# Optimization experiments

Measured on AMD Instinct MI355X. Metric: run time of the kernel, lower is better.

The kernel has to match this reference:

```python
import jax, jax.numpy as jnp
import numpy as np

KERNEL_MUL = 2.0
KERNEL_NUM = 5


def _index_matrix(b: int) -> jnp.ndarray:
    # non-linear JMMD index matrix (linear=False)
    im = np.zeros((2 * b, 2 * b), dtype=np.float32)
    off = 1.0 / float(b * (b - 1))
    eye = np.eye(b, dtype=bool)
    im[:b, :b][~eye] = off
    im[b:, b:][~eye] = off
    im[:b, b:] = -1.0 / float(b * b)
    im[b:, :b] = -1.0 / float(b * b)
    return jnp.asarray(im)


def _gaussian_kernel(source, target):
    total = jnp.concatenate([source, target], axis=0)  # [2b, d]
    n = total.shape[0]
    sq = jnp.sum(total * total, axis=1)  # [2b]
    # pairwise squared L2 via Gram matrix (same math as expand/diff/sum)
    l2 = sq[:, None] + sq[None, :] - 2.0 * (total @ total.T)
    l2 = jnp.maximum(l2, 0.0)
    # bandwidth computed on detached distances (torch uses .data)
    bw = jax.lax.stop_gradient(jnp.sum(l2)) / float(n * n - n)
    bw = bw / (KERNEL_MUL ** (KERNEL_NUM // 2))
    k = jnp.zeros_like(l2)
    for i in range(KERNEL_NUM):
        k = k + jnp.exp(-l2 / (bw * (KERNEL_MUL ** i)))
    return k


def setup_inputs() -> dict:
    key = jax.random.key(0)
    k1, k2, k3, k4 = jax.random.split(key, 4)
    b, d1, d2 = 2048, 4096, 2048
    return {
        "z1_s": jax.random.normal(k1, (b, d1), dtype=jnp.float32),
        "z1_t": jax.random.normal(k2, (b, d1), dtype=jnp.float32),
        "z2_s": jax.random.normal(k3, (b, d2), dtype=jnp.float32),
        "z2_t": jax.random.normal(k4, (b, d2), dtype=jnp.float32),
    }


def reference(z1_s, z1_t, z2_s, z2_t):
    b = z1_s.shape[0]
    index_matrix = _index_matrix(b)  # [2b, 2b]
    kernel_matrix = _gaussian_kernel(z1_s, z1_t) * _gaussian_kernel(z2_s, z2_t)
    loss = jnp.sum(kernel_matrix * index_matrix) + 2.0 / float(b - 1)
    return loss
```

## Files before the change

### kernel.cpp

```cpp
#include <hip/hip_runtime.h>
#include <cstdint>

#define NTOT 4096
#define BHALF 2048
#define D1 4096
#define D2 2048
#define TT 32
#define NTILES 528

typedef __attribute__((ext_vector_type(4))) float f32x4;
typedef __attribute__((ext_vector_type(4))) int i32x4;
typedef __attribute__((ext_vector_type(8))) int i32x8;

__device__ __forceinline__ void glds16(const uint8_t* g, uint8_t* l) {
    __builtin_amdgcn_global_load_lds(
        (const __attribute__((address_space(1))) void*)(uintptr_t)g,
        (__attribute__((address_space(3))) void*)(uint32_t)(uintptr_t)l,
        16, 0, 0);
}

__device__ __forceinline__ i32x4 ldsr(uint32_t addr) {
    i32x4 r;
    asm volatile("ds_read_b128 %0, %1" : "=v"(r) : "v"(addr));
    return r;
}

__device__ __forceinline__ float fp8dec(unsigned b) {
    unsigned e = (b >> 3) & 15u, m = b & 7u;
    float v = e ? __uint_as_float(((e + 120u) << 23) | (m << 20))
                : (float)m * 0.001953125f;
    return (b & 128u) ? -v : v;
}

__global__ void prep_kernel(const float* __restrict__ z1s, const float* __restrict__ z1t,
                            const float* __restrict__ z2s, const float* __restrict__ z2t,
                            float* __restrict__ sq1, float* __restrict__ sq2,
                            uint8_t* __restrict__ t1f8, uint8_t* __restrict__ t2f8,
                            float* __restrict__ s1, float* __restrict__ s2,
                            unsigned* __restrict__ ctrl, float* __restrict__ out) {
    int bid = blockIdx.x;
    int tid = threadIdx.x;
    if (bid == 0) { for (int i = tid; i < 4096; i += 256) s1[i] = 0.f; }
    if (bid == 1) { for (int i = tid; i < 2048; i += 256) s2[i] = 0.f; }
    if (bid == 2) {
        if (tid < 4) ctrl[tid] = 0u;
        if (tid == 4) out[0] = 2.0f / (float)(BHALF - 1);
    }
    int which = bid >> 12;
    int row = bid & 4095;
    int d = which ? D2 : D1;
    const float* s_ = which ? z2s : z1s;
    const float* t_ = which ? z2t : z1t;
    const float* src = (row < BHALF) ? s_ + (size_t)row * d : t_ + (size_t)(row - BHALF) * d;
    uint8_t* dst = (which ? t2f8 : t1f8) + (size_t)row * d;
    float* sq = which ? sq2 : sq1;
    const float4* src4 = (const float4*)src;
    float a = 0.f;
    int n8 = d >> 3;
    for (int i = tid; i < n8; i += 256) {
        float4 v0 = src4[2 * i], v1 = src4[2 * i + 1];
        a += v0.x * v0.x + v0.y * v0.y + v0.z * v0.z + v0.w * v0.w;
        a += v1.x * v1.x + v1.y * v1.y + v1.z * v1.z + v1.w * v1.w;
        int w0 = __builtin_amdgcn_cvt_pk_fp8_f32(v0.x, v0.y, 0, 0);
        w0 = __builtin_amdgcn_cvt_pk_fp8_f32(v0.z, v0.w, w0, 1);
        int w1 = __builtin_amdgcn_cvt_pk_fp8_f32(v1.x, v1.y, 0, 0);
        w1 = __builtin_amdgcn_cvt_pk_fp8_f32(v1.z, v1.w, w1, 1);
        ((uint2*)dst)[i] = uint2{(unsigned)w0, (unsigned)w1};
    }
    for (int o = 32; o; o >>= 1) a += __shfl_down(a, o);
    __shared__ float sh[4];
    int lane = tid & 63, w = tid >> 6;
    if (lane == 0) sh[w] = a;
    __syncthreads();
    if (tid == 0) sq[row] = sh[0] + sh[1] + sh[2] + sh[3];
}

__device__ __forceinline__ void gemm_mx_pipe(const uint8_t* __restrict__ ga,
                                             const uint8_t* __restrict__ gb,
                                             int d,
                                             uint8_t* A0, uint8_t* B0,
                                             uint8_t* A1, uint8_t* B1,
                                             f32x4 (&acc)[4][4], int wv, int lane,
                                             int wm, int wn, int lm, int quad) {
    int nsteps = d >> 7;
    int rsub = lane >> 3;
    int ql = (lane & 7) ^ rsub;
    const uint8_t* pa = ga + (size_t)(wv * 32 + rsub) * d + ql * 16;
    const uint8_t* pb = gb + (size_t)(wv * 32 + rsub) * d + ql * 16;
    uint8_t* dA[2] = { A0 + wv * 4096, A1 + wv * 4096 };
    uint8_t* dB[2] = { B0 + wv * 4096, B1 + wv * 4096 };
    uint32_t baseA[2] = { (uint32_t)(uintptr_t)A0, (uint32_t)(uintptr_t)A1 };
    uint32_t baseB[2] = { (uint32_t)(uintptr_t)B0, (uint32_t)(uintptr_t)B1 };
    int s0 = ((2 * quad) ^ (lm & 7)) * 16;
    int s1 = ((2 * quad + 1) ^ (lm & 7)) * 16;
    uint32_t offA[4], offB[4];
#pragma unroll
    for (int i = 0; i < 4; ++i) {
        offA[i] = (uint32_t)((wm * 64 + i * 16 + lm) * 128);
        offB[i] = (uint32_t)((wn * 64 + i * 16 + lm) * 128);
    }
#pragma unroll
    for (int i = 0; i < 4; ++i) {
        glds16(pa + (size_t)i * 8 * d, dA[0] + i * 1024);
        glds16(pb + (size_t)i * 8 * d, dB[0] + i * 1024);
    }
    for (int k = 0; k < nsteps; ++k) {
        int cur = k & 1, nxt = cur ^ 1;
        size_t koff = (size_t)((k + 1 < nsteps) ? (k + 1) : 0) << 7;
#pragma unroll
        for (int i = 0; i < 4; ++i) {
            glds16(pa + koff + (size_t)i * 8 * d, dA[nxt] + i * 1024);
            glds16(pb + koff + (size_t)i * 8 * d, dB[nxt] + i * 1024);
        }
        asm volatile("s_waitcnt vmcnt(8)\n\ts_barrier" ::: "memory");
        i32x4 b00 = ldsr(baseB[cur] + offB[0] + s0), b01 = ldsr(baseB[cur] + offB[0] + s1);
        i32x4 b10 = ldsr(baseB[cur] + offB[1] + s0), b11 = ldsr(baseB[cur] + offB[1] + s1);
        i32x4 a00 = ldsr(baseA[cur] + offA[0] + s0), a01 = ldsr(baseA[cur] + offA[0] + s1);
        i32x4 a10 = ldsr(baseA[cur] + offA[1] + s0), a11 = ldsr(baseA[cur] + offA[1] + s1);
        i32x4 b20 = ldsr(baseB[cur] + offB[2] + s0), b21 = ldsr(baseB[cur] + offB[2] + s1);
        i32x4 b30 = ldsr(baseB[cur] + offB[3] + s0), b31 = ldsr(baseB[cur] + offB[3] + s1);
        i32x4 a20 = ldsr(baseA[cur] + offA[2] + s0), a21 = ldsr(baseA[cur] + offA[2] + s1);
        i32x4 a30 = ldsr(baseA[cur] + offA[3] + s0), a31 = ldsr(baseA[cur] + offA[3] + s1);
        union F { i32x4 h[2]; i32x8 v; };
        F ua0, ua1, ua2, ua3, ub0, ub1, ub2, ub3;
        asm volatile("s_waitcnt lgkmcnt(8)"
                     : "+v"(b00), "+v"(b01), "+v"(b10), "+v"(b11),
                       "+v"(a00), "+v"(a01), "+v"(a10), "+v"(a11));
        __builtin_amdgcn_sched_barrier(0);
        ub0.h[0] = b00; ub0.h[1] = b01; ub1.h[0] = b10; ub1.h[1] = b11;
        ua0.h[0] = a00; ua0.h[1] = a01; ua1.h[0] = a10; ua1.h[1] = a11;
        __builtin_amdgcn_s_setprio(1);
        acc[0][0] = __builtin_amdgcn_mfma_scale_f32_16x16x128_f8f6f4(ua0.v, ub0.v, acc[0][0], 0, 0, 0, 0x7F7F7F7F, 0, 0x7F7F7F7F);
        acc[0][1] = __builtin_amdgcn_mfma_scale_f32_16x16x128_f8f6f4(ua0.v, ub1.v, acc[0][1], 0, 0, 0, 0x7F7F7F7F, 0, 0x7F7F7F7F);
        acc[1][0] = __builtin_amdgcn_mfma_scale_f32_16x16x128_f8f6f4(ua1.v, ub0.v, acc[1][0], 0, 0, 0, 0x7F7F7F7F, 0, 0x7F7F7F7F);
        acc[1][1] = __builtin_amdgcn_mfma_scale_f32_16x16x128_f8f6f4(ua1.v, ub1.v, acc[1][1], 0, 0, 0, 0x7F7F7F7F, 0, 0x7F7F7F7F);
        __builtin_amdgcn_s_setprio(0);
        asm volatile("s_waitcnt lgkmcnt(4)"
                     : "+v"(b20), "+v"(b21), "+v"(b30), "+v"(b31));
        __builtin_amdgcn_sched_barrier(0);
        ub2.h[0] = b20; ub2.h[1] = b21; ub3.h[0] = b30; ub3.h[1] = b31;
        __builtin_amdgcn_s_setprio(1);
        acc[0][2] = __builtin_amdgcn_mfma_scale_f32_16x16x128_f8f6f4(ua0.v, ub2.v, acc[0][2], 0, 0, 0, 0x7F7F7F7F, 0, 0x7F7F7F7F);
        acc[0][3] = __builtin_amdgcn_mfma_scale_f32_16x16x128_f8f6f4(ua0.v, ub3.v, acc[0][3], 0, 0, 0, 0x7F7F7F7F, 0, 0x7F7F7F7F);
        acc[1][2] = __builtin_amdgcn_mfma_scale_f32_16x16x128_f8f6f4(ua1.v, ub2.v, acc[1][2], 0, 0, 0, 0x7F7F7F7F, 0, 0x7F7F7F7F);
        acc[1][3] = __builtin_amdgcn_mfma_scale_f32_16x16x128_f8f6f4(ua1.v, ub3.v, acc[1][3], 0, 0, 0, 0x7F7F7F7F, 0, 0x7F7F7F7F);
        __builtin_amdgcn_s_setprio(0);
        asm volatile("s_waitcnt lgkmcnt(0)"
                     : "+v"(a20), "+v"(a21), "+v"(a30), "+v"(a31));
        __builtin_amdgcn_sched_barrier(0);
        asm volatile("s_barrier" ::: "memory");
        __builtin_amdgcn_sched_barrier(0);
        ua2.h[0] = a20; ua2.h[1] = a21; ua3.h[0] = a30; ua3.h[1] = a31;
        __builtin_amdgcn_s_setprio(1);
        acc[2][0] = __builtin_amdgcn_mfma_scale_f32_16x16x128_f8f6f4(ua2.v, ub0.v, acc[2][0], 0, 0, 0, 0x7F7F7F7F, 0, 0x7F7F7F7F);
        acc[2][1] = __builtin_amdgcn_mfma_scale_f32_16x16x128_f8f6f4(ua2.v, ub1.v, acc[2][1], 0, 0, 0, 0x7F7F7F7F, 0, 0x7F7F7F7F);
        acc[2][2] = __builtin_amdgcn_mfma_scale_f32_16x16x128_f8f6f4(ua2.v, ub2.v, acc[2][2], 0, 0, 0, 0x7F7F7F7F, 0, 0x7F7F7F7F);
        acc[2][3] = __builtin_amdgcn_mfma_scale_f32_16x16x128_f8f6f4(ua2.v, ub3.v, acc[2][3], 0, 0, 0, 0x7F7F7F7F, 0, 0x7F7F7F7F);
        acc[3][0] = __builtin_amdgcn_mfma_scale_f32_16x16x128_f8f6f4(ua3.v, ub0.v, acc[3][0], 0, 0, 0, 0x7F7F7F7F, 0, 0x7F7F7F7F);
        acc[3][1] = __builtin_amdgcn_mfma_scale_f32_16x16x128_f8f6f4(ua3.v, ub1.v, acc[3][1], 0, 0, 0, 0x7F7F7F7F, 0, 0x7F7F7F7F);
        acc[3][2] = __builtin_amdgcn_mfma_scale_f32_16x16x128_f8f6f4(ua3.v, ub2.v, acc[3][2], 0, 0, 0, 0x7F7F7F7F, 0, 0x7F7F7F7F);
        acc[3][3] = __builtin_amdgcn_mfma_scale_f32_16x16x128_f8f6f4(ua3.v, ub3.v, acc[3][3], 0, 0, 0, 0x7F7F7F7F, 0, 0x7F7F7F7F);
        __builtin_amdgcn_s_setprio(0);
    }
}

__global__ __launch_bounds__(256, 2) void jmmd_fused(
    const uint8_t* __restrict__ t1f8, const uint8_t* __restrict__ t2f8,
    const float* __restrict__ sq1, const float* __restrict__ sq2,
    float* __restrict__ s1v, float* __restrict__ s2v,
    unsigned* __restrict__ ctrl, float* __restrict__ out) {
    __shared__ alignas(16) uint8_t smem[4][16384];
    int tid = threadIdx.x;
    int bid = blockIdx.x;

    if (bid < 384) {
        int which = bid >= 256;
        int local = which ? bid - 256 : bid;
        int d = which ? D2 : D1;
        int colchunks = d >> 10;
        int cb = local % colchunks, rb = local / colchunks;
        const uint8_t* base = which ? t2f8 : t1f8;
        float* s = which ? s2v : s1v;
        int col = (cb << 10) + tid * 4;
        const uint8_t* p = base + (size_t)(rb * 64) * d + col;
        float a0 = 0.f, a1 = 0.f, a2 = 0.f, a3 = 0.f;
#pragma unroll 4
        for (int r = 0; r < 64; ++r) {
            uchar4 u = *(const uchar4*)(p + (size_t)r * d);
            a0 += fp8dec(u.x); a1 += fp8dec(u.y); a2 += fp8dec(u.z); a3 += fp8dec(u.w);
        }
        atomicAdd(&s[col], a0); atomicAdd(&s[col + 1], a1);
        atomicAdd(&s[col + 2], a2); atomicAdd(&s[col + 3], a3);
        __threadfence();
        __syncthreads();
        unsigned* rkp = (unsigned*)(smem[0] + 64);
        if (tid == 0) *rkp = atomicAdd(&ctrl[0], 1u);
        __syncthreads();
        unsigned rk = *rkp;
        __syncthreads();
        if (rk == 383u) {
            float a1_ = 0.f, a2_ = 0.f, q1_ = 0.f, q2_ = 0.f;
            for (int i = tid; i < 4096; i += 256) {
                float v = __uint_as_float(atomicOr((unsigned*)&s1v[i], 0u));
                a1_ += v * v; q1_ += sq1[i]; q2_ += sq2[i];
            }
            for (int i = tid; i < 2048; i += 256) {
                float v = __uint_as_float(atomicOr((unsigned*)&s2v[i], 0u));
                a2_ += v * v;
            }
            for (int o = 32; o; o >>= 1) {
                a1_ += __shfl_down(a1_, o); a2_ += __shfl_down(a2_, o);
                q1_ += __shfl_down(q1_, o); q2_ += __shfl_down(q2_, o);
            }
            float* fsh = (float*)smem[0];
            int lane = tid & 63, w = tid >> 6;
            if (lane == 0) { fsh[0 * 4 + w] = a1_; fsh[1 * 4 + w] = a2_; fsh[2 * 4 + w] = q1_; fsh[3 * 4 + w] = q2_; }
            __syncthreads();
            if (tid == 0) {
                double ss1 = (double)fsh[0] + fsh[1] + fsh[2] + fsh[3];
                double ss2 = (double)fsh[4] + fsh[5] + fsh[6] + fsh[7];
                double t1 = (double)fsh[8] + fsh[9] + fsh[10] + fsh[11];
                double t2 = (double)fsh[12] + fsh[13] + fsh[14] + fsh[15];
                double S1 = 2.0 * (double)NTOT * t1 - 2.0 * ss1;
                double S2 = 2.0 * (double)NTOT * t2 - 2.0 * ss2;
                const double L2E = 1.4426950408889634;
                double nn = (double)NTOT * (double)(NTOT - 1);
                atomicExch(&ctrl[2], __float_as_uint((float)(nn * L2E / (4.0 * S1))));
                atomicExch(&ctrl[3], __float_as_uint((float)(nn * L2E / (4.0 * S2))));
                __threadfence();
                atomicExch(&ctrl[1], 1u);
            }
            __syncthreads();
        }
    }

    int ti = 0, r = bid;
    while (r >= TT - ti) { r -= TT - ti; ++ti; }
    int tj = ti + r;
    int i0 = ti * 128, j0 = tj * 128;
    int lane = tid & 63, wv = tid >> 6;
    int wm = wv >> 1, wn = wv & 1, lm = lane & 15, quad = lane >> 4;
    f32x4 acc1[4][4] = {};
    f32x4 acc2[4][4] = {};
    gemm_mx_pipe(t1f8 + (size_t)i0 * D1, t1f8 + (size_t)j0 * D1, D1,
                 smem[0], smem[1], smem[2], smem[3], acc1, wv, lane, wm, wn, lm, quad);
    asm volatile("s_waitcnt vmcnt(0)\n\ts_barrier" ::: "memory");
    gemm_mx_pipe(t2f8 + (size_t)i0 * D2, t2f8 + (size_t)j0 * D2, D2,
                 smem[0], smem[1], smem[2], smem[3], acc2, wv, lane, wm, wn, lm, quad);
    asm volatile("s_waitcnt vmcnt(0)" ::: "memory");
    __syncthreads();

    float* cvp = (float*)smem[1];
    if (tid == 0) {
        while (atomicOr(&ctrl[1], 0u) == 0u) __builtin_amdgcn_s_sleep(8);
        cvp[0] = __uint_as_float(atomicOr(&ctrl[2], 0u));
        cvp[1] = __uint_as_float(atomicOr(&ctrl[3], 0u));
    }
    __syncthreads();
    float c1 = cvp[0], c2 = cvp[1];
    float local = 0.f;
    bool diag = (ti == tj);
#pragma unroll
    for (int mi = 0; mi < 4; ++mi) {
        int rbase = wm * 64 + mi * 16 + quad * 4;
#pragma unroll
        for (int ni = 0; ni < 4; ++ni) {
            int col = wn * 64 + ni * 16 + lm;
            float sb1 = sq1[j0 + col], sb2 = sq2[j0 + col];
#pragma unroll
            for (int rr = 0; rr < 4; ++rr) {
                int row = rbase + rr;
                float l2a = fmaxf(sq1[i0 + row] + sb1 - 2.f * acc1[mi][ni][rr], 0.f);
                float l2b = fmaxf(sq2[i0 + row] + sb2 - 2.f * acc2[mi][ni][rr], 0.f);
                float t1 = __builtin_amdgcn_exp2f(-l2a * c1);
                float k1 = t1; float u1 = t1 * t1; k1 += u1; u1 *= u1; k1 += u1; u1 *= u1; k1 += u1; u1 *= u1; k1 += u1;
                float t2 = __builtin_amdgcn_exp2f(-l2b * c2);
                float k2 = t2; float u2 = t2 * t2; k2 += u2; u2 *= u2; k2 += u2; u2 *= u2; k2 += u2; u2 *= u2; k2 += u2;
                float v = k1 * k2;
                if (diag && (row == col)) v = 0.f;
                local += v;
            }
        }
    }
    for (int o = 32; o; o >>= 1) local += __shfl_down(local, o);
    float* redp = (float*)smem[0];
    if (lane == 0) redp[wv] = local;
    __syncthreads();
    if (tid == 0) {
        bool same = (i0 < BHALF) == (j0 < BHALF);
        float w = same ? (1.0f / ((float)BHALF * (float)(BHALF - 1)))
                       : (-1.0f / ((float)BHALF * (float)BHALF));
        if (!diag) w *= 2.f;
        atomicAdd(out, (redp[0] + redp[1] + redp[2] + redp[3]) * w);
    }
}

extern "C" void kernel_launch(void* const* d_in, const int* in_sizes, int n_in,
                              void* d_out, int out_size, void* d_ws, size_t ws_size,
                              hipStream_t stream) {
    const float* z1s = (const float*)d_in[0];
    const float* z1t = (const float*)d_in[1];
    const float* z2s = (const float*)d_in[2];
    const float* z2t = (const float*)d_in[3];
    float* out = (float*)d_out;

    float* ws = (float*)d_ws;
    float* sq1 = ws;
    float* sq2 = ws + 4096;
    float* s1  = ws + 8192;
    float* s2  = ws + 12288;
    unsigned* ctrl = (unsigned*)(ws + 14336);
    uint8_t* t1f8 = (uint8_t*)(ws + 14344);
    uint8_t* t2f8 = t1f8 + (size_t)NTOT * D1;

    prep_kernel<<<8192, 256, 0, stream>>>(z1s, z1t, z2s, z2t, sq1, sq2, t1f8, t2f8, s1, s2, ctrl, out);
    jmmd_fused<<<NTILES, 256, 0, stream>>>(t1f8, t2f8, sq1, sq2, s1, s2, ctrl, out);
}
```

Measured before the change: 296.6 us.

## Split column-sum bandwidth stage into separate kernel and unroll prep loops

Moves the column-sum and bandwidth-finalization work out of the fused GEMM kernel into its own 384-block kernel launched between prep and GEMM. This removes the spin-wait on a global flag in every GEMM block and the extra work in the first 384 tiles, at the cost of an additional kernel launch and a serialized stage. The prep kernel loop is also fully unrolled per row width, with launch bounds raised to allow more resident blocks.

New measurement: 284.4 us. 1.04x faster.

```diff
diff --git a/kernel.cpp b/kernel.cpp
--- a/kernel.cpp
+++ b/kernel.cpp
@@ -32,47 +32,119 @@
     return (b & 128u) ? -v : v;
 }
 
-__global__ void prep_kernel(const float* __restrict__ z1s, const float* __restrict__ z1t,
-                            const float* __restrict__ z2s, const float* __restrict__ z2t,
-                            float* __restrict__ sq1, float* __restrict__ sq2,
-                            uint8_t* __restrict__ t1f8, uint8_t* __restrict__ t2f8,
-                            float* __restrict__ s1, float* __restrict__ s2,
-                            unsigned* __restrict__ ctrl, float* __restrict__ out) {
+__device__ __forceinline__ int cvt2fp8(float4 v) {
+    int w = __builtin_amdgcn_cvt_pk_fp8_f32(v.x, v.y, 0, 0);
+    return __builtin_amdgcn_cvt_pk_fp8_f32(v.z, v.w, w, 1);
+}
+
+__global__ __launch_bounds__(256, 4) void prep_kernel(
+        const float* __restrict__ z1s, const float* __restrict__ z1t,
+        const float* __restrict__ z2s, const float* __restrict__ z2t,
+        float* __restrict__ sq1, float* __restrict__ sq2,
+        uint8_t* __restrict__ t1f8, uint8_t* __restrict__ t2f8,
+        float* __restrict__ s1, float* __restrict__ s2,
+        unsigned* __restrict__ ctrl, float* __restrict__ out) {
     int bid = blockIdx.x;
     int tid = threadIdx.x;
     if (bid == 0) { for (int i = tid; i < 4096; i += 256) s1[i] = 0.f; }
     if (bid == 1) { for (int i = tid; i < 2048; i += 256) s2[i] = 0.f; }
     if (bid == 2) {
-        if (tid < 4) ctrl[tid] = 0u;
-        if (tid == 4) out[0] = 2.0f / (float)(BHALF - 1);
+        if (tid == 0) ctrl[0] = 0u;
+        if (tid == 1) out[0] = 2.0f / (float)(BHALF - 1);
     }
     int which = bid >> 12;
     int row = bid & 4095;
-    int d = which ? D2 : D1;
-    const float* s_ = which ? z2s : z1s;
-    const float* t_ = which ? z2t : z1t;
-    const float* src = (row < BHALF) ? s_ + (size_t)row * d : t_ + (size_t)(row - BHALF) * d;
-    uint8_t* dst = (which ? t2f8 : t1f8) + (size_t)row * d;
-    float* sq = which ? sq2 : sq1;
-    const float4* src4 = (const float4*)src;
     float a = 0.f;
-    int n8 = d >> 3;
-    for (int i = tid; i < n8; i += 256) {
-        float4 v0 = src4[2 * i], v1 = src4[2 * i + 1];
-        a += v0.x * v0.x + v0.y * v0.y + v0.z * v0.z + v0.w * v0.w;
-        a += v1.x * v1.x + v1.y * v1.y + v1.z * v1.z + v1.w * v1.w;
-        int w0 = __builtin_amdgcn_cvt_pk_fp8_f32(v0.x, v0.y, 0, 0);
-        w0 = __builtin_amdgcn_cvt_pk_fp8_f32(v0.z, v0.w, w0, 1);
-        int w1 = __builtin_amdgcn_cvt_pk_fp8_f32(v1.x, v1.y, 0, 0);
-        w1 = __builtin_amdgcn_cvt_pk_fp8_f32(v1.z, v1.w, w1, 1);
-        ((uint2*)dst)[i] = uint2{(unsigned)w0, (unsigned)w1};
+    if (which == 0) {
+        const float* src = (row < BHALF) ? z1s + (size_t)row * D1
+                                         : z1t + (size_t)(row - BHALF) * D1;
+        uint8_t* dst = t1f8 + (size_t)row * D1;
+        const float4* s4 = (const float4*)src;
+        float4 p0 = s4[2 * tid], p1 = s4[2 * tid + 1];
+        float4 p2 = s4[2 * tid + 512], p3 = s4[2 * tid + 513];
+        a += p0.x * p0.x + p0.y * p0.y + p0.z * p0.z + p0.w * p0.w;
+        a += p1.x * p1.x + p1.y * p1.y + p1.z * p1.z + p1.w * p1.w;
+        a += p2.x * p2.x + p2.y * p2.y + p2.z * p2.z + p2.w * p2.w;
+        a += p3.x * p3.x + p3.y * p3.y + p3.z * p3.z + p3.w * p3.w;
+        ((uint2*)dst)[tid]       = uint2{(unsigned)cvt2fp8(p0), (unsigned)cvt2fp8(p1)};
+        ((uint2*)dst)[tid + 256] = uint2{(unsigned)cvt2fp8(p2), (unsigned)cvt2fp8(p3)};
+    } else {
+        const float* src = (row < BHALF) ? z2s + (size_t)row * D2
+                                         : z2t + (size_t)(row - BHALF) * D2;
+        uint8_t* dst = t2f8 + (size_t)row * D2;
+        const float4* s4 = (const float4*)src;
+        float4 p0 = s4[2 * tid], p1 = s4[2 * tid + 1];
+        a += p0.x * p0.x + p0.y * p0.y + p0.z * p0.z + p0.w * p0.w;
+        a += p1.x * p1.x + p1.y * p1.y + p1.z * p1.z + p1.w * p1.w;
+        ((uint2*)dst)[tid] = uint2{(unsigned)cvt2fp8(p0), (unsigned)cvt2fp8(p1)};
     }
     for (int o = 32; o; o >>= 1) a += __shfl_down(a, o);
     __shared__ float sh[4];
     int lane = tid & 63, w = tid >> 6;
     if (lane == 0) sh[w] = a;
     __syncthreads();
-    if (tid == 0) sq[row] = sh[0] + sh[1] + sh[2] + sh[3];
+    if (tid == 0) (which ? sq2 : sq1)[row] = sh[0] + sh[1] + sh[2] + sh[3];
+}
+
+__global__ void colsum_fin_kernel(const uint8_t* __restrict__ t1f8,
+                                  const uint8_t* __restrict__ t2f8,
+                                  float* __restrict__ s1, float* __restrict__ s2,
+                                  const float* __restrict__ sq1, const float* __restrict__ sq2,
+                                  unsigned* __restrict__ ctrl, float* __restrict__ acc) {
+    int bid = blockIdx.x;
+    int tid = threadIdx.x;
+    int which = bid >= 256;
+    int local = which ? bid - 256 : bid;
+    int d = which ? D2 : D1;
+    int colchunks = d >> 10;
+    int cb = local % colchunks, rb = local / colchunks;
+    const uint8_t* base = which ? t2f8 : t1f8;
+    float* s = which ? s2 : s1;
+    int col = (cb << 10) + tid * 4;
+    const uint8_t* p = base + (size_t)(rb * 64) * d + col;
+    float a0 = 0.f, a1 = 0.f, a2 = 0.f, a3 = 0.f;
+#pragma unroll 4
+    for (int r = 0; r < 64; ++r) {
+        uchar4 u = *(const uchar4*)(p + (size_t)r * d);
+        a0 += fp8dec(u.x); a1 += fp8dec(u.y); a2 += fp8dec(u.z); a3 += fp8dec(u.w);
+    }
+    atomicAdd(&s[col], a0); atomicAdd(&s[col + 1], a1);
+    atomicAdd(&s[col + 2], a2); atomicAdd(&s[col + 3], a3);
+    __threadfence();
+    __syncthreads();
+    __shared__ unsigned rk_sh;
+    __shared__ float fsh[16];
+    if (tid == 0) rk_sh = atomicAdd(&ctrl[0], 1u);
+    __syncthreads();
+    if (rk_sh != 383u) return;
+    float a1_ = 0.f, a2_ = 0.f, q1_ = 0.f, q2_ = 0.f;
+    for (int i = tid; i < 4096; i += 256) {
+        float v = __uint_as_float(atomicOr((unsigned*)&s1[i], 0u));
+        a1_ += v * v; q1_ += sq1[i]; q2_ += sq2[i];
+    }
+    for (int i = tid; i < 2048; i += 256) {
+        float v = __uint_as_float(atomicOr((unsigned*)&s2[i], 0u));
+        a2_ += v * v;
+    }
+    for (int o = 32; o; o >>= 1) {
+        a1_ += __shfl_down(a1_, o); a2_ += __shfl_down(a2_, o);
+        q1_ += __shfl_down(q1_, o); q2_ += __shfl_down(q2_, o);
+    }
+    int lane = tid & 63, w = tid >> 6;
+    if (lane == 0) { fsh[0 + w] = a1_; fsh[4 + w] = a2_; fsh[8 + w] = q1_; fsh[12 + w] = q2_; }
+    __syncthreads();
+    if (tid == 0) {
+        double ss1 = (double)fsh[0] + fsh[1] + fsh[2] + fsh[3];
+        double ss2 = (double)fsh[4] + fsh[5] + fsh[6] + fsh[7];
+        double t1 = (double)fsh[8] + fsh[9] + fsh[10] + fsh[11];
+        double t2 = (double)fsh[12] + fsh[13] + fsh[14] + fsh[15];
+        double S1 = 2.0 * (double)NTOT * t1 - 2.0 * ss1;
+        double S2 = 2.0 * (double)NTOT * t2 - 2.0 * ss2;
+        const double L2E = 1.4426950408889634;
+        double nn = (double)NTOT * (double)(NTOT - 1);
+        acc[2] = (float)(nn * L2E / (4.0 * S1));
+        acc[3] = (float)(nn * L2E / (4.0 * S2));
+    }
 }
 
 __device__ __forceinline__ void gemm_mx_pipe(const uint8_t* __restrict__ ga,
@@ -167,74 +239,10 @@
 __global__ __launch_bounds__(256, 2) void jmmd_fused(
     const uint8_t* __restrict__ t1f8, const uint8_t* __restrict__ t2f8,
     const float* __restrict__ sq1, const float* __restrict__ sq2,
-    float* __restrict__ s1v, float* __restrict__ s2v,
-    unsigned* __restrict__ ctrl, float* __restrict__ out) {
+    const float* __restrict__ cv, float* __restrict__ out) {
     __shared__ alignas(16) uint8_t smem[4][16384];
     int tid = threadIdx.x;
-    int bid = blockIdx.x;
-
-    if (bid < 384) {
-        int which = bid >= 256;
-        int local = which ? bid - 256 : bid;
-        int d = which ? D2 : D1;
-        int colchunks = d >> 10;
-        int cb = local % colchunks, rb = local / colchunks;
-        const uint8_t* base = which ? t2f8 : t1f8;
-        float* s = which ? s2v : s1v;
-        int col = (cb << 10) + tid * 4;
-        const uint8_t* p = base + (size_t)(rb * 64) * d + col;
-        float a0 = 0.f, a1 = 0.f, a2 = 0.f, a3 = 0.f;
-#pragma unroll 4
-        for (int r = 0; r < 64; ++r) {
-            uchar4 u = *(const uchar4*)(p + (size_t)r * d);
-            a0 += fp8dec(u.x); a1 += fp8dec(u.y); a2 += fp8dec(u.z); a3 += fp8dec(u.w);
-        }
-        atomicAdd(&s[col], a0); atomicAdd(&s[col + 1], a1);
-        atomicAdd(&s[col + 2], a2); atomicAdd(&s[col + 3], a3);
-        __threadfence();
-        __syncthreads();
-        unsigned* rkp = (unsigned*)(smem[0] + 64);
-        if (tid == 0) *rkp = atomicAdd(&ctrl[0], 1u);
-        __syncthreads();
-        unsigned rk = *rkp;
-        __syncthreads();
-        if (rk == 383u) {
-            float a1_ = 0.f, a2_ = 0.f, q1_ = 0.f, q2_ = 0.f;
-            for (int i = tid; i < 4096; i += 256) {
-                float v = __uint_as_float(atomicOr((unsigned*)&s1v[i], 0u));
-                a1_ += v * v; q1_ += sq1[i]; q2_ += sq2[i];
-            }
-            for (int i = tid; i < 2048; i += 256) {
-                float v = __uint_as_float(atomicOr((unsigned*)&s2v[i], 0u));
-                a2_ += v * v;
-            }
-            for (int o = 32; o; o >>= 1) {
-                a1_ += __shfl_down(a1_, o); a2_ += __shfl_down(a2_, o);
-                q1_ += __shfl_down(q1_, o); q2_ += __shfl_down(q2_, o);
-            }
-            float* fsh = (float*)smem[0];
-            int lane = tid & 63, w = tid >> 6;
-            if (lane == 0) { fsh[0 * 4 + w] = a1_; fsh[1 * 4 + w] = a2_; fsh[2 * 4 + w] = q1_; fsh[3 * 4 + w] = q2_; }
-            __syncthreads();
-            if (tid == 0) {
-                double ss1 = (double)fsh[0] + fsh[1] + fsh[2] + fsh[3];
-                double ss2 = (double)fsh[4] + fsh[5] + fsh[6] + fsh[7];
-                double t1 = (double)fsh[8] + fsh[9] + fsh[10] + fsh[11];
-                double t2 = (double)fsh[12] + fsh[13] + fsh[14] + fsh[15];
-                double S1 = 2.0 * (double)NTOT * t1 - 2.0 * ss1;
-                double S2 = 2.0 * (double)NTOT * t2 - 2.0 * ss2;
-                const double L2E = 1.4426950408889634;
-                double nn = (double)NTOT * (double)(NTOT - 1);
-                atomicExch(&ctrl[2], __float_as_uint((float)(nn * L2E / (4.0 * S1))));
-                atomicExch(&ctrl[3], __float_as_uint((float)(nn * L2E / (4.0 * S2))));
-                __threadfence();
-                atomicExch(&ctrl[1], 1u);
-            }
-            __syncthreads();
-        }
-    }
-
-    int ti = 0, r = bid;
+    int ti = 0, r = blockIdx.x;
     while (r >= TT - ti) { r -= TT - ti; ++ti; }
     int tj = ti + r;
     int i0 = ti * 128, j0 = tj * 128;
@@ -249,15 +257,7 @@
                  smem[0], smem[1], smem[2], smem[3], acc2, wv, lane, wm, wn, lm, quad);
     asm volatile("s_waitcnt vmcnt(0)" ::: "memory");
     __syncthreads();
-
-    float* cvp = (float*)smem[1];
-    if (tid == 0) {
-        while (atomicOr(&ctrl[1], 0u) == 0u) __builtin_amdgcn_s_sleep(8);
-        cvp[0] = __uint_as_float(atomicOr(&ctrl[2], 0u));
-        cvp[1] = __uint_as_float(atomicOr(&ctrl[3], 0u));
-    }
-    __syncthreads();
-    float c1 = cvp[0], c2 = cvp[1];
+    float c1 = cv[0], c2 = cv[1];
     float local = 0.f;
     bool diag = (ti == tj);
 #pragma unroll
@@ -309,10 +309,12 @@
     float* sq2 = ws + 4096;
     float* s1  = ws + 8192;
     float* s2  = ws + 12288;
-    unsigned* ctrl = (unsigned*)(ws + 14336);
+    float* acc = ws + 14336;
+    unsigned* ctrl = (unsigned*)(ws + 14340);
     uint8_t* t1f8 = (uint8_t*)(ws + 14344);
     uint8_t* t2f8 = t1f8 + (size_t)NTOT * D1;
 
     prep_kernel<<<8192, 256, 0, stream>>>(z1s, z1t, z2s, z2t, sq1, sq2, t1f8, t2f8, s1, s2, ctrl, out);
-    jmmd_fused<<<NTILES, 256, 0, stream>>>(t1f8, t2f8, sq1, sq2, s1, s2, ctrl, out);
-}
+    colsum_fin_kernel<<<384, 256, 0, stream>>>(t1f8, t2f8, s1, s2, sq1, sq2, ctrl, acc);
+    jmmd_fused<<<NTILES, 256, 0, stream>>>(t1f8, t2f8, sq1, sq2, acc + 2, out);
+}
```
